# Kernel tuning notes

Measured on AMD Instinct MI355X. Metric: run time of the kernel, lower is better.

## Reference

```python
import jax, jax.numpy as jnp
import numpy as np
from jax import lax

INPUT_DIM = 1024
HIDDEN_DIM = 2048
N, L = 64, 512


def setup_inputs() -> dict:
    key = jax.random.key(0)
    ks = jax.random.split(key, 6)
    X = jax.random.normal(ks[0], (N, L, INPUT_DIM), dtype=jnp.float32)
    H0 = jnp.zeros((N, HIDDEN_DIM), dtype=jnp.float32)
    # G-invariant layer params (DeepSets invariant map): out = w * sum(x) + b, one per gate (i,f,g,o)
    inv_scale = 1.0 / np.sqrt(INPUT_DIM)
    inv_w = jax.random.normal(ks[1], (4, HIDDEN_DIM), dtype=jnp.float32) * inv_scale
    inv_b = jax.random.normal(ks[2], (4, HIDDEN_DIM), dtype=jnp.float32) * inv_scale
    # Linear(hidden, hidden) per gate, torch convention W: (out, in)
    lin_scale = 1.0 / np.sqrt(HIDDEN_DIM)
    lin_W = jax.random.normal(ks[3], (4, HIDDEN_DIM, HIDDEN_DIM), dtype=jnp.float32) * lin_scale
    lin_b = jax.random.normal(ks[4], (4, HIDDEN_DIM), dtype=jnp.float32) * lin_scale
    return {"X": X, "H0": H0, "inv_w": inv_w, "inv_b": inv_b, "lin_W": lin_W, "lin_b": lin_b}


def reference(X, H0, inv_w, inv_b, lin_W, lin_b):
    # X: (N, L, D); H0: (N, H)
    def step(carry, x_t):
        h, c = carry                               # (N, H), (N, H)
        s = jnp.sum(x_t, axis=-1, keepdims=True)   # (N, 1) invariant statistic
        inv = s * inv_w[:, None, :] + inv_b[:, None, :]            # (4, N, H)
        lin = jnp.einsum('nh,gkh->gnk', h, lin_W) + lin_b[:, None, :]  # (4, N, H)
        z = inv + lin
        i = jax.nn.sigmoid(z[0])
        f = jax.nn.sigmoid(z[1])
        g = jnp.tanh(z[2])
        o = jax.nn.sigmoid(z[3])
        c = f * c + i * g
        h = o * jnp.tanh(c)
        return (h, c), None

    Xt = jnp.swapaxes(X, 0, 1)                     # (L, N, D)
    (h, _), _ = lax.scan(step, (H0, jnp.zeros_like(H0)), Xt)
    # original returns swapdims(hidden_state, 0, 1) -> (H, N)
    return h.T
```

## Files before the change

### kernel.cpp

```cpp
#include <hip/hip_runtime.h>
#include <hip/hip_fp16.h>


typedef _Float16 f16x8 __attribute__((ext_vector_type(8)));
typedef float    f32x4 __attribute__((ext_vector_type(4)));
typedef unsigned long long u64;

#define LROW 2056
#define NBLK 256u

static __device__ __forceinline__ float fast_sig(float x) {
  return 1.f / (1.f + __expf(-x));
}
static __device__ __forceinline__ float fast_tanh(float x) {
  x = fminf(15.f, fmaxf(-15.f, x));
  const float e = __expf(2.f * x);
  return (e - 1.f) / (e + 1.f);
}

static __device__ __forceinline__ void st_h16(void* p, float v) {
  const unsigned short b = __builtin_bit_cast(unsigned short, (_Float16)v);
  __hip_atomic_store((unsigned short*)p, b, __ATOMIC_RELAXED, __HIP_MEMORY_SCOPE_AGENT);
}
static __device__ __forceinline__ void st_h64(void* p, u64 v) {
  __hip_atomic_store((u64*)p, v, __ATOMIC_RELAXED, __HIP_MEMORY_SCOPE_AGENT);
}

static __device__ __forceinline__ int h_off(int n, int j) {
  return ((n >> 4) << 16) + ((j >> 5) << 10) + ((n & 15) << 6) +
         (((j >> 3) & 3) << 4) + ((j & 7) << 1);
}

__global__ void __launch_bounds__(256) seq_sum_kernel(const float* __restrict__ X,
                                                      float* s_all) {
  const int gw   = (int)((blockIdx.x * blockDim.x + threadIdx.x) >> 6);
  const int lane = threadIdx.x & 63;
  const int n = gw >> 9, t = gw & 511;
  const float4* p = (const float4*)(X + ((size_t)gw << 10));
  float s = 0.f;
#pragma unroll
  for (int i = 0; i < 4; ++i) {
    const float4 v = p[lane + (i << 6)];
    s += (v.x + v.y) + (v.z + v.w);
  }
#pragma unroll
  for (int off = 32; off; off >>= 1) s += __shfl_xor(s, off);
  if (lane == 0) s_all[(t << 6) + n] = s;
}

__global__ void bar_init_kernel(unsigned* bar) {
  bar[threadIdx.x]       = 0u;
  bar[threadIdx.x + 256] = 0u;
  bar[threadIdx.x + 512] = 0u;
  bar[threadIdx.x + 768] = 0u;
}

static __device__ __forceinline__ void grid_barrier2(unsigned* bar, unsigned round,
                                                     int tid, int blk) {
  asm volatile("s_waitcnt vmcnt(0)" ::: "memory");
  __syncthreads();
  if (tid == 0) {
    unsigned* grp  = bar + ((blk & 7) << 5);
    unsigned* root = bar + 512;
    const unsigned old =
        __hip_atomic_fetch_add(grp, 1u, __ATOMIC_RELAXED, __HIP_MEMORY_SCOPE_AGENT);
    if (old == 32u * round - 1u)
      __hip_atomic_fetch_add(root, 1u, __ATOMIC_RELAXED, __HIP_MEMORY_SCOPE_AGENT);
    const unsigned target = 8u * round;
    unsigned guard = 0;
    while (__hip_atomic_load(root, __ATOMIC_RELAXED, __HIP_MEMORY_SCOPE_AGENT) <
           target) {
      __builtin_amdgcn_s_sleep(1);
      if (++guard > (1u << 23)) break;
    }
  }
  __syncthreads();
}

#define LOAD4(d0, d1, d2, d3, addr)                                         \
  asm volatile("global_load_dwordx4 %0, %4, off sc1\n\t"                    \
               "global_load_dwordx4 %1, %4, off offset:1024 sc1\n\t"        \
               "global_load_dwordx4 %2, %4, off offset:2048 sc1\n\t"        \
               "global_load_dwordx4 %3, %4, off offset:3072 sc1"            \
               : "=v"(d0), "=v"(d1), "=v"(d2), "=v"(d3)                     \
               : "v"(addr)                                                  \
               : "memory")

#define WAITG(n, A)                                                         \
  asm volatile("s_waitcnt vmcnt(" #n ")"                                    \
               : "+v"(A[0]), "+v"(A[1]), "+v"(A[2]), "+v"(A[3]),            \
                 "+v"(A[4]), "+v"(A[5]), "+v"(A[6]), "+v"(A[7]),            \
                 "+v"(A[8]), "+v"(A[9]), "+v"(A[10]), "+v"(A[11]),          \
                 "+v"(A[12]), "+v"(A[13]), "+v"(A[14]), "+v"(A[15])         \
               :                                                            \
               : "memory")

__global__ void __launch_bounds__(256, 1) ginv_lstm_persist(
    const float* __restrict__ lin_W, const float* __restrict__ inv_w,
    const float* __restrict__ inv_b, const float* __restrict__ lin_b,
    const float* s_all, const float* __restrict__ H0,
    _Float16* hb0, _Float16* hb1, unsigned* bar, float* out) {
  __shared__ _Float16 Wl[32 * LROW];
  __shared__ __align__(16) _Float16 hx[64][8];
  const int blk = blockIdx.x;
  const int tid = threadIdx.x;
  _Float16* hbuf[2] = {hb0, hb1};

  for (int base = tid * 4; base < 32 * 2048; base += 1024) {
    const int r  = base >> 11;
    const int hc = base & 2047;
    const int g  = r >> 3;
    const int kf = r & 7;
    const float4 v =
        *(const float4*)&lin_W[(((size_t)(g * 2048 + blk * 8 + kf)) << 11) + hc];
    _Float16* d = &Wl[r * LROW + hc];
    d[0] = (_Float16)v.x; d[1] = (_Float16)v.y;
    d[2] = (_Float16)v.z; d[3] = (_Float16)v.w;
  }

  {
    int i0 = blk * 512 + tid;
    st_h16((char*)hb0 + h_off(i0 >> 11, i0 & 2047), H0[i0]);
    i0 += 256;
    st_h16((char*)hb0 + h_off(i0 >> 11, i0 & 2047), H0[i0]);
  }

  const int wave = tid >> 6;
  const int lane = tid & 63;
  const int q    = lane >> 4;
  const int cc   = lane & 15;
  const int kf   = cc & 7;
  const int Kg   = blk * 8 + kf;
  const int g0   = (cc < 8) ? 0 : 1;
  const int g1   = (cc < 8) ? 2 : 3;
  const float w0 = inv_w[(g0 << 11) + Kg];
  const float b0 = inv_b[(g0 << 11) + Kg] + lin_b[(g0 << 11) + Kg];
  const float w1 = inv_w[(g1 << 11) + Kg];
  const float b1 = inv_b[(g1 << 11) + Kg] + lin_b[(g1 << 11) + Kg];

  unsigned round = 1;
  grid_barrier2(bar, round, tid, blk);

  float cst[4] = {0.f, 0.f, 0.f, 0.f};

  const int ld_base = (wave << 16) + (cc << 6) + (q << 4);
  const int lb0 = cc * LROW + q * 8;
  const int lb1 = (16 + cc) * LROW + q * 8;
  const int st_off = ((lane >> 4) << 16) + ((blk >> 2) << 10) + ((lane & 15) << 6) +
                     ((blk & 3) << 4);

  for (int t = 0; t < 512; ++t) {
    const char* hpb = (const char*)hbuf[t & 1] + ld_base;

    const float4 s4 = *(const float4*)&s_all[(t << 6) + wave * 16 + q * 4];

    f16x8 pa[16], pb[16];

#pragma unroll
    for (int w = 0; w < 4; ++w)
      LOAD4(pa[w * 4], pa[w * 4 + 1], pa[w * 4 + 2], pa[w * 4 + 3],
            hpb + (w << 12));
#pragma unroll
    for (int w = 0; w < 4; ++w)
      LOAD4(pb[w * 4], pb[w * 4 + 1], pb[w * 4 + 2], pb[w * 4 + 3],
            hpb + 16384 + (w << 12));

    f32x4 acc0 = {0.f, 0.f, 0.f, 0.f};
    f32x4 acc1 = {0.f, 0.f, 0.f, 0.f};

    auto kmath = [&](const f16x8* A, int gbase) {
#pragma unroll
      for (int i = 0; i < 16; ++i) {
        const int kc = gbase + i;
        const f16x8 bb0 = *(const f16x8*)&Wl[lb0 + kc * 32];
        const f16x8 bb1 = *(const f16x8*)&Wl[lb1 + kc * 32];
        acc0 = __builtin_amdgcn_mfma_f32_16x16x32_f16(A[i], bb0, acc0, 0, 0, 0);
        acc1 = __builtin_amdgcn_mfma_f32_16x16x32_f16(A[i], bb1, acc1, 0, 0, 0);
      }
    };

    WAITG(16, pa);
    kmath(pa, 0);
#pragma unroll
    for (int w = 0; w < 4; ++w)
      LOAD4(pa[w * 4], pa[w * 4 + 1], pa[w * 4 + 2], pa[w * 4 + 3],
            hpb + 32768 + (w << 12));
    WAITG(16, pb);
    kmath(pb, 16);
#pragma unroll
    for (int w = 0; w < 4; ++w)
      LOAD4(pb[w * 4], pb[w * 4 + 1], pb[w * 4 + 2], pb[w * 4 + 3],
            hpb + 49152 + (w << 12));
    WAITG(16, pa);
    kmath(pa, 32);
    WAITG(0, pb);
    kmath(pb, 48);

    const float sv[4] = {s4.x, s4.y, s4.z, s4.w};
    float hnew[4];
#pragma unroll
    for (int v = 0; v < 4; ++v) {
      const float z0 = acc0[v] + sv[v] * w0 + b0;
      const float z1 = acc1[v] + sv[v] * w1 + b1;
      const float zf = __shfl_xor(z0, 8);
      const float zo = __shfl_xor(z1, 8);
      const float ig = fast_sig(z0);
      const float fg = fast_sig(zf);
      const float gg = fast_tanh(z1);
      const float og = fast_sig(zo);
      const float cn = fg * cst[v] + ig * gg;
      cst[v] = cn;
      hnew[v] = og * fast_tanh(cn);
    }

    if (cc < 8) {
#pragma unroll
      for (int v = 0; v < 4; ++v)
        hx[(wave << 4) + (q << 2) + v][cc] = (_Float16)hnew[v];
    }
    __syncthreads();
    if (t < 511 && tid < 64) {
      union { f16x8 v; u64 w[2]; } u;
      u.v = *(const f16x8*)hx[lane];
      char* dst = (char*)hbuf[(t + 1) & 1] + st_off;
      st_h64(dst, u.w[0]);
      st_h64(dst + 8, u.w[1]);
    }
    ++round;
    grid_barrier2(bar, round, tid, blk);
  }

  if (tid < 64) {
    const f16x8 hv = *(const f16x8*)hx[lane];
#pragma unroll
    for (int f = 0; f < 8; ++f)
      out[((blk * 8 + f) << 6) + lane] = (float)hv[f];
  }
}

extern "C" void kernel_launch(void* const* d_in, const int* in_sizes, int n_in,
                              void* d_out, int out_size, void* d_ws, size_t ws_size,
                              hipStream_t stream) {
  const float* X     = (const float*)d_in[0];
  const float* H0    = (const float*)d_in[1];
  const float* inv_w = (const float*)d_in[2];
  const float* inv_b = (const float*)d_in[3];
  const float* lin_W = (const float*)d_in[4];
  const float* lin_b = (const float*)d_in[5];
  float* out = (float*)d_out;

  const size_t S_BYTES = 512 * 64 * 4;
  const size_t BAR_PAD = 4096;
  const size_t H_BYTES = 64 * 2048 * 2;
  const size_t NEED = S_BYTES + BAR_PAD + 2 * H_BYTES;

  float*    s_all;
  unsigned* bar;
  _Float16* hb[2];
  if (ws_size >= NEED) {
    char* ws = (char*)d_ws;
    s_all = (float*)ws;
    bar   = (unsigned*)(ws + S_BYTES);
    for (int i = 0; i < 2; ++i)
      hb[i] = (_Float16*)(ws + S_BYTES + BAR_PAD + (size_t)i * H_BYTES);
  } else {
    s_all = (float*)d_out;
    char* xt = (char*)d_in[0] + (size_t)64 * 512 * 1024 * 4 -
               (BAR_PAD + 2 * H_BYTES);
    bar = (unsigned*)xt;
    for (int i = 0; i < 2; ++i)
      hb[i] = (_Float16*)(xt + BAR_PAD + (size_t)i * H_BYTES);
  }

  seq_sum_kernel<<<8192, 256, 0, stream>>>(X, s_all);
  bar_init_kernel<<<1, 256, 0, stream>>>(bar);
  ginv_lstm_persist<<<256, 256, 0, stream>>>(lin_W, inv_w, inv_b, lin_b, s_all, H0,
                                             hb[0], hb[1], bar, out);
}
```

Measured before the change: 4.285 ms.

## Keep weights in registers and split K across waves with LDS reduction

Each wave now holds its slice of the fp16 weight tile in registers and covers a quarter of the hidden dimension for all 64 batch rows, instead of covering 16 batch rows over the full K with weights read from LDS every step. Partial sums are reduced through a swizzled shared-memory buffer, and each lane then computes all four gates for its batch element and two hidden units. This removes the per-step LDS weight reads but adds a per-step reduction, an extra __syncthreads, and high register pressure from 32 weight vectors plus 8 accumulators.

```diff
diff --git a/kernel.cpp b/kernel.cpp
--- a/kernel.cpp
+++ b/kernel.cpp
@@ -5,9 +5,6 @@
 typedef _Float16 f16x8 __attribute__((ext_vector_type(8)));
 typedef float    f32x4 __attribute__((ext_vector_type(4)));
 typedef unsigned long long u64;
-
-#define LROW 2056
-#define NBLK 256u
 
 static __device__ __forceinline__ float fast_sig(float x) {
   return 1.f / (1.f + __expf(-x));
@@ -95,27 +92,49 @@
                :                                                            \
                : "memory")
 
+#define KMATH(A, bt)                                                        \
+  _Pragma("unroll")                                                         \
+  for (int i_ = 0; i_ < 16; ++i_) {                                         \
+    acc[bt][0] = __builtin_amdgcn_mfma_f32_16x16x32_f16(A[i_], Wr[i_][0],   \
+                                                        acc[bt][0], 0, 0, 0); \
+    acc[bt][1] = __builtin_amdgcn_mfma_f32_16x16x32_f16(A[i_], Wr[i_][1],   \
+                                                        acc[bt][1], 0, 0, 0); \
+  }
+
 __global__ void __launch_bounds__(256, 1) ginv_lstm_persist(
     const float* __restrict__ lin_W, const float* __restrict__ inv_w,
     const float* __restrict__ inv_b, const float* __restrict__ lin_b,
     const float* s_all, const float* __restrict__ H0,
     _Float16* hb0, _Float16* hb1, unsigned* bar, float* out) {
-  __shared__ _Float16 Wl[32 * LROW];
+  __shared__ float red[12][64][32];
   __shared__ __align__(16) _Float16 hx[64][8];
   const int blk = blockIdx.x;
   const int tid = threadIdx.x;
   _Float16* hbuf[2] = {hb0, hb1};
 
-  for (int base = tid * 4; base < 32 * 2048; base += 1024) {
-    const int r  = base >> 11;
-    const int hc = base & 2047;
-    const int g  = r >> 3;
-    const int kf = r & 7;
-    const float4 v =
-        *(const float4*)&lin_W[(((size_t)(g * 2048 + blk * 8 + kf)) << 11) + hc];
-    _Float16* d = &Wl[r * LROW + hc];
-    d[0] = (_Float16)v.x; d[1] = (_Float16)v.y;
-    d[2] = (_Float16)v.z; d[3] = (_Float16)v.w;
+  const int wave = tid >> 6;
+  const int lane = tid & 63;
+  const int q    = lane >> 4;
+  const int cc   = lane & 15;
+
+  f16x8 Wr[16][2];
+#pragma unroll
+  for (int ct = 0; ct < 2; ++ct) {
+    const int c  = ct * 16 + cc;
+    const int kf = c >> 2, g = c & 3;
+    const float* wrow =
+        lin_W + (((size_t)(g * 2048 + blk * 8 + kf)) << 11) + wave * 512 + q * 8;
+#pragma unroll
+    for (int kc = 0; kc < 16; ++kc) {
+      const float4 va = *(const float4*)(wrow + kc * 32);
+      const float4 vb = *(const float4*)(wrow + kc * 32 + 4);
+      f16x8 f;
+      f[0] = (_Float16)va.x; f[1] = (_Float16)va.y;
+      f[2] = (_Float16)va.z; f[3] = (_Float16)va.w;
+      f[4] = (_Float16)vb.x; f[5] = (_Float16)vb.y;
+      f[6] = (_Float16)vb.z; f[7] = (_Float16)vb.w;
+      Wr[kc][ct] = f;
+    }
   }
 
   {
@@ -125,34 +144,30 @@
     st_h16((char*)hb0 + h_off(i0 >> 11, i0 & 2047), H0[i0]);
   }
 
-  const int wave = tid >> 6;
-  const int lane = tid & 63;
-  const int q    = lane >> 4;
-  const int cc   = lane & 15;
-  const int kf   = cc & 7;
-  const int Kg   = blk * 8 + kf;
-  const int g0   = (cc < 8) ? 0 : 1;
-  const int g1   = (cc < 8) ? 2 : 3;
-  const float w0 = inv_w[(g0 << 11) + Kg];
-  const float b0 = inv_b[(g0 << 11) + Kg] + lin_b[(g0 << 11) + Kg];
-  const float w1 = inv_w[(g1 << 11) + Kg];
-  const float b1 = inv_b[(g1 << 11) + Kg] + lin_b[(g1 << 11) + Kg];
+  float iw[2][4], ibb[2][4];
+#pragma unroll
+  for (int kk = 0; kk < 2; ++kk) {
+    const int Kg = blk * 8 + wave + (kk << 2);
+#pragma unroll
+    for (int g = 0; g < 4; ++g) {
+      iw[kk][g]  = inv_w[(g << 11) + Kg];
+      ibb[kk][g] = inv_b[(g << 11) + Kg] + lin_b[(g << 11) + Kg];
+    }
+  }
 
   unsigned round = 1;
   grid_barrier2(bar, round, tid, blk);
 
-  float cst[4] = {0.f, 0.f, 0.f, 0.f};
-
-  const int ld_base = (wave << 16) + (cc << 6) + (q << 4);
-  const int lb0 = cc * LROW + q * 8;
-  const int lb1 = (16 + cc) * LROW + q * 8;
+  float cst[2] = {0.f, 0.f};
+
+  const int ld_base = (wave << 14) + (cc << 6) + (q << 4);
   const int st_off = ((lane >> 4) << 16) + ((blk >> 2) << 10) + ((lane & 15) << 6) +
                      ((blk & 3) << 4);
 
   for (int t = 0; t < 512; ++t) {
     const char* hpb = (const char*)hbuf[t & 1] + ld_base;
 
-    const float4 s4 = *(const float4*)&s_all[(t << 6) + wave * 16 + q * 4];
+    const float sv = s_all[(t << 6) + lane];
 
     f16x8 pa[16], pb[16];
 
@@ -163,61 +178,67 @@
 #pragma unroll
     for (int w = 0; w < 4; ++w)
       LOAD4(pb[w * 4], pb[w * 4 + 1], pb[w * 4 + 2], pb[w * 4 + 3],
-            hpb + 16384 + (w << 12));
-
-    f32x4 acc0 = {0.f, 0.f, 0.f, 0.f};
-    f32x4 acc1 = {0.f, 0.f, 0.f, 0.f};
-
-    auto kmath = [&](const f16x8* A, int gbase) {
-#pragma unroll
-      for (int i = 0; i < 16; ++i) {
-        const int kc = gbase + i;
-        const f16x8 bb0 = *(const f16x8*)&Wl[lb0 + kc * 32];
-        const f16x8 bb1 = *(const f16x8*)&Wl[lb1 + kc * 32];
-        acc0 = __builtin_amdgcn_mfma_f32_16x16x32_f16(A[i], bb0, acc0, 0, 0, 0);
-        acc1 = __builtin_amdgcn_mfma_f32_16x16x32_f16(A[i], bb1, acc1, 0, 0, 0);
-      }
-    };
+            hpb + 65536 + (w << 12));
+
+    f32x4 acc[4][2];
+#pragma unroll
+    for (int bt = 0; bt < 4; ++bt)
+#pragma unroll
+      for (int ct = 0; ct < 2; ++ct) acc[bt][ct] = (f32x4){0.f, 0.f, 0.f, 0.f};
 
     WAITG(16, pa);
-    kmath(pa, 0);
+    KMATH(pa, 0);
 #pragma unroll
     for (int w = 0; w < 4; ++w)
       LOAD4(pa[w * 4], pa[w * 4 + 1], pa[w * 4 + 2], pa[w * 4 + 3],
-            hpb + 32768 + (w << 12));
+            hpb + 131072 + (w << 12));
     WAITG(16, pb);
-    kmath(pb, 16);
+    KMATH(pb, 1);
 #pragma unroll
     for (int w = 0; w < 4; ++w)
       LOAD4(pb[w * 4], pb[w * 4 + 1], pb[w * 4 + 2], pb[w * 4 + 3],
-            hpb + 49152 + (w << 12));
+            hpb + 196608 + (w << 12));
     WAITG(16, pa);
-    kmath(pa, 32);
+    KMATH(pa, 2);
     WAITG(0, pb);
-    kmath(pb, 48);
-
-    const float sv[4] = {s4.x, s4.y, s4.z, s4.w};
-    float hnew[4];
-#pragma unroll
-    for (int v = 0; v < 4; ++v) {
-      const float z0 = acc0[v] + sv[v] * w0 + b0;
-      const float z1 = acc1[v] + sv[v] * w1 + b1;
-      const float zf = __shfl_xor(z0, 8);
-      const float zo = __shfl_xor(z1, 8);
-      const float ig = fast_sig(z0);
+    KMATH(pb, 3);
+
+#pragma unroll
+    for (int bt = 0; bt < 4; ++bt)
+#pragma unroll
+      for (int ct = 0; ct < 2; ++ct) {
+        const int c = ct * 16 + cc;
+#pragma unroll
+        for (int v = 0; v < 4; ++v) {
+          const int n = bt * 16 + (q << 2) + v;
+          red[wave][n][(((c >> 2) ^ (n & 7)) << 2) + (c & 3)] = acc[bt][ct][v];
+        }
+      }
+    __syncthreads();
+
+    float hnew[2];
+#pragma unroll
+    for (int kk = 0; kk < 2; ++kk) {
+      const int kf  = wave + (kk << 2);
+      const int off = (kf ^ (lane & 7)) << 2;
+      f32x4 zz = *(const f32x4*)&red[0][lane][off];
+#pragma unroll
+      for (int w = 1; w < 4; ++w) zz += *(const f32x4*)&red[w][lane][off];
+      const float zi = zz[0] + sv * iw[kk][0] + ibb[kk][0];
+      const float zf = zz[1] + sv * iw[kk][1] + ibb[kk][1];
+      const float zg = zz[2] + sv * iw[kk][2] + ibb[kk][2];
+      const float zo = zz[3] + sv * iw[kk][3] + ibb[kk][3];
+      const float ig = fast_sig(zi);
       const float fg = fast_sig(zf);
-      const float gg = fast_tanh(z1);
+      const float gg = fast_tanh(zg);
       const float og = fast_sig(zo);
-      const float cn = fg * cst[v] + ig * gg;
-      cst[v] = cn;
-      hnew[v] = og * fast_tanh(cn);
-    }
-
-    if (cc < 8) {
-#pragma unroll
-      for (int v = 0; v < 4; ++v)
-        hx[(wave << 4) + (q << 2) + v][cc] = (_Float16)hnew[v];
-    }
+      const float cn = fg * cst[kk] + ig * gg;
+      cst[kk] = cn;
+      hnew[kk] = og * fast_tanh(cn);
+    }
+
+    hx[lane][wave]     = (_Float16)hnew[0];
+    hx[lane][wave + 4] = (_Float16)hnew[1];
     __syncthreads();
     if (t < 511 && tid < 64) {
       union { f16x8 v; u64 w[2]; } u;
```

Measured after the change: 4.252 ms. Within noise of the previous version (-0.8%).
